# Kernel optimization log

Hardware: AMD Instinct MI355X
Metric: run time of the kernel (lower is better)

## Reference

```python
import jax, jax.numpy as jnp
import numpy as np

N_CUST = 500000
N_FUND = 50000
N_EDGE = 4000000
D_CUST = 101
D_FUND = 1
HID = 64


def setup_inputs() -> dict:
    key = jax.random.key(0)
    ks = jax.random.split(key, 16)
    s = lambda fan_in: 1.0 / np.sqrt(fan_in)
    return {
        "x_customer": jax.random.normal(ks[0], (N_CUST, D_CUST), jnp.float32),
        "x_fund": jax.random.normal(ks[1], (N_FUND, D_FUND), jnp.float32),
        "src_fund": jax.random.randint(ks[2], (N_EDGE,), 0, N_FUND, jnp.int64),
        "dst_customer": jax.random.randint(ks[3], (N_EDGE,), 0, N_CUST, jnp.int64),
        # per-node-type input projections
        "W_cust": jax.random.uniform(ks[4], (D_CUST, HID), jnp.float32, -s(D_CUST), s(D_CUST)),
        "b_cust": jax.random.uniform(ks[5], (HID,), jnp.float32, -s(D_CUST), s(D_CUST)),
        "W_fund": jax.random.uniform(ks[6], (D_FUND, HID), jnp.float32, -s(D_FUND), s(D_FUND)),
        "b_fund": jax.random.uniform(ks[7], (HID,), jnp.float32, -s(D_FUND), s(D_FUND)),
        # SAGEConv fund->customer: lin_l (neighbor aggr, bias) + lin_r (self, no bias)
        "W_l": jax.random.uniform(ks[8], (HID, HID), jnp.float32, -s(HID), s(HID)),
        "b_l": jax.random.uniform(ks[9], (HID,), jnp.float32, -s(HID), s(HID)),
        "W_r": jax.random.uniform(ks[10], (HID, HID), jnp.float32, -s(HID), s(HID)),
        # output head
        "W_out": jax.random.uniform(ks[11], (HID, 2), jnp.float32, -s(HID), s(HID)),
        "b_out": jax.random.uniform(ks[12], (2,), jnp.float32, -s(HID), s(HID)),
    }


def reference(x_customer, x_fund, src_fund, dst_customer,
              W_cust, b_cust, W_fund, b_fund, W_l, b_l, W_r, W_out, b_out):
    # per-node-type linear + relu
    h_c = jax.nn.relu(x_customer @ W_cust + b_cust)  # [N_CUST, HID]
    h_f = jax.nn.relu(x_fund @ W_fund + b_fund)      # [N_FUND, HID]

    # SAGEConv (fund -> customer): gather src fund features per edge,
    # mean-aggregate by destination customer (scatter-sum / count)
    msgs = h_f[src_fund]  # [N_EDGE, HID]
    summed = jax.ops.segment_sum(msgs, dst_customer, num_segments=N_CUST)
    cnt = jax.ops.segment_sum(jnp.ones((msgs.shape[0],), msgs.dtype),
                              dst_customer, num_segments=N_CUST)
    mean = summed / jnp.maximum(cnt, 1.0)[:, None]

    out_c = mean @ W_l + b_l + h_c @ W_r  # SAGE: lin_l(aggr) + lin_r(self)
    return out_c @ W_out + b_out          # [N_CUST, 2]
```

## Files before the change

kernel.cpp:

```cpp
#include <hip/hip_runtime.h>
#include <stdint.h>

#define N_CUST 500000
#define N_FUND 50000
#define N_EDGE 4000000
#define D_CUST 101
#define HID 64

#define NB   512
#define EPB  ((N_EDGE + NB - 1) / NB)
#define CB   1024
#define NBKT ((N_CUST + CB - 1) / CB)
#define CAP  16384
#define TILES (N_CUST / 16)

typedef float  float4u __attribute__((ext_vector_type(4), aligned(4)));
using frag_ab = __attribute__((ext_vector_type(8))) short;
using frag_cd = __attribute__((ext_vector_type(4))) float;

struct __align__(16) Accum { float g0, g1, cnt, pad; };

__device__ __forceinline__ short f2bf(float f) {
    unsigned u = __float_as_uint(f);
    u += 0x7fffu + ((u >> 16) & 1u);
    return (short)(u >> 16);
}

__global__ __launch_bounds__(256) void k_prep(
    const float* __restrict__ W_r, const float* __restrict__ W_out,
    const float* __restrict__ b_l, const float* __restrict__ b_out,
    const float* __restrict__ W_l,
    float* __restrict__ Bt, float* __restrict__ Af, float* __restrict__ c2,
    unsigned* __restrict__ gcur)
{
    int t = threadIdx.x;
    if (t < 128) {
        int h = t >> 1, j = t & 1;
        float s = 0.f, sa = 0.f;
        for (int k = 0; k < 64; ++k) {
            float wo = W_out[k * 2 + j];
            s  = fmaf(W_r[h * 64 + k], wo, s);
            sa = fmaf(W_l[h * 64 + k], wo, sa);
        }
        Bt[t] = s;
        Af[t] = sa;
    } else if (t < 130) {
        int j = t - 128;
        float s = b_out[j];
        for (int k = 0; k < 64; ++k)
            s = fmaf(b_l[k], W_out[k * 2 + j], s);
        c2[j] = s;
    }
    for (int k = t; k < NBKT; k += 256) gcur[k] = (unsigned)k * CAP;
}

__global__ __launch_bounds__(256) void k_gf(
    const float* __restrict__ x_fund,
    const float* __restrict__ W_fund,
    const float* __restrict__ b_fund,
    const float* __restrict__ Af,
    float2* __restrict__ gf)
{
    int f = blockIdx.x * 256 + threadIdx.x;
    if (f >= N_FUND) return;
    float xf = x_fund[f];
    float g0 = 0.f, g1 = 0.f;
    #pragma unroll
    for (int h = 0; h < 64; ++h) {
        float hf = fmaxf(fmaf(xf, W_fund[h], b_fund[h]), 0.f);
        g0 = fmaf(hf, Af[2 * h + 0], g0);
        g1 = fmaf(hf, Af[2 * h + 1], g1);
    }
    gf[f] = make_float2(g0, g1);
}

__global__ __launch_bounds__(256) void k_reorder(
    const int* __restrict__ src, const int* __restrict__ dst,
    unsigned* __restrict__ gcur, unsigned* __restrict__ recs)
{
    __shared__ unsigned hist[NBKT];
    __shared__ unsigned localOff[NBKT];
    __shared__ unsigned cur[NBKT];
    __shared__ unsigned baseG[NBKT];
    __shared__ unsigned ldsRec[EPB];
    __shared__ unsigned short ldsBkt[EPB];

    int t = threadIdx.x, b = blockIdx.x;
    int e0 = b * EPB, e1 = min(e0 + EPB, N_EDGE);
    int cntE = e1 - e0;

    for (int k = t; k < NBKT; k += 256) hist[k] = 0;
    __syncthreads();
    for (int e = e0 + t; e < e1; e += 256)
        atomicAdd(&hist[((unsigned)dst[e]) >> 10], 1u);
    __syncthreads();

    if (t < 64) {
        unsigned v[8], pre[8], run = 0;
        #pragma unroll
        for (int j = 0; j < 8; ++j) {
            int idx = t * 8 + j;
            v[j] = (idx < NBKT) ? hist[idx] : 0u;
            pre[j] = run; run += v[j];
        }
        unsigned sc = run;
        #pragma unroll
        for (int d = 1; d < 64; d <<= 1) {
            unsigned n = __shfl_up(sc, d, 64);
            if (t >= d) sc += n;
        }
        unsigned lane_excl = sc - run;
        #pragma unroll
        for (int j = 0; j < 8; ++j) {
            int idx = t * 8 + j;
            if (idx < NBKT) {
                localOff[idx] = lane_excl + pre[j];
                cur[idx]      = lane_excl + pre[j];
            }
        }
    }
    __syncthreads();

    for (int k = t; k < NBKT; k += 256) {
        unsigned h = hist[k];
        baseG[k] = h ? atomicAdd(&gcur[k], h) : 0u;
    }

    for (int e = e0 + t; e < e1; e += 256) {
        unsigned d = (unsigned)dst[e];
        unsigned s = (unsigned)src[e];
        unsigned k = d >> 10;
        unsigned p = atomicAdd(&cur[k], 1u);
        ldsRec[p] = s | ((d & 1023u) << 16);
        ldsBkt[p] = (unsigned short)k;
    }
    __syncthreads();

    for (int i = t; i < cntE; i += 256) {
        unsigned k = ldsBkt[i];
        unsigned g = baseG[k] + (i - localOff[k]);
        recs[g] = ldsRec[i];
    }
}

__global__ __launch_bounds__(256) void k_aggregate(
    const unsigned* __restrict__ recs, const unsigned* __restrict__ gcur,
    const float2* __restrict__ gf, float2* __restrict__ mean)
{
    __shared__ float s0[CB], s1[CB], scn[CB];
    int t = threadIdx.x, k = blockIdx.x;
    for (int c = t; c < CB; c += 256) { s0[c] = 0.f; s1[c] = 0.f; scn[c] = 0.f; }
    __syncthreads();
    unsigned r0 = (unsigned)k * CAP, r1 = gcur[k];
    for (unsigned i = r0 + t; i < r1; i += 256) {
        unsigned r = recs[i];
        float2 g = gf[r & 0xFFFFu];
        unsigned dl = r >> 16;
        atomicAdd(&s0[dl], g.x);
        atomicAdd(&s1[dl], g.y);
        atomicAdd(&scn[dl], 1.f);
    }
    __syncthreads();
    int cust0 = k * CB;
    for (int c = t; c < CB; c += 256) {
        int cu = cust0 + c;
        if (cu < N_CUST) {
            float inv = 1.0f / fmaxf(scn[c], 1.0f);
            mean[cu] = make_float2(s0[c] * inv, s1[c] * inv);
        }
    }
}

__global__ __launch_bounds__(256) void k_scatter_direct(
    const int* __restrict__ src, const int* __restrict__ dst,
    const float2* __restrict__ gf, Accum* __restrict__ A)
{
    int stride = gridDim.x * 256;
    for (int e = blockIdx.x * 256 + threadIdx.x; e < N_EDGE; e += stride) {
        int s = src[e], d = dst[e];
        float2 g = gf[s];
        unsafeAtomicAdd(&A[d].g0, g.x);
        unsafeAtomicAdd(&A[d].g1, g.y);
        unsafeAtomicAdd(&A[d].cnt, 1.0f);
    }
}

template<bool USE_MEAN>
__global__ __launch_bounds__(256) void k_cust(
    const float* __restrict__ x, const float* __restrict__ Wc,
    const float* __restrict__ bc, const float* __restrict__ Bt,
    const float* __restrict__ c2,
    const float2* __restrict__ mean, const Accum* __restrict__ A,
    float2* __restrict__ out)
{
    __shared__ float zb[4][16 * 68];
    __shared__ float sBt[128];
    int tid = threadIdx.x;
    int w = tid >> 6, lane = tid & 63;
    int c = lane & 15, q = lane >> 4;
    float* z = zb[w];

    if (tid < 128) sBt[tid] = Bt[tid];

    frag_ab bfrag[4][4];
    for (int nt = 0; nt < 4; ++nt)
        for (int kc = 0; kc < 4; ++kc) {
            frag_ab f;
            for (int j = 0; j < 8; ++j) {
                int k = kc * 32 + q * 8 + j;
                int h = nt * 16 + c;
                f[j] = (k < D_CUST) ? f2bf(Wc[k * HID + h]) : (short)0;
            }
            bfrag[nt][kc] = f;
        }
    float bcv[4];
    #pragma unroll
    for (int nt = 0; nt < 4; ++nt) bcv[nt] = bc[nt * 16 + c];
    float c20 = c2[0], c21 = c2[1];
    __syncthreads();

    int wglob = blockIdx.x * 4 + w;
    int wstride = gridDim.x * 4;
    for (int t = wglob; t < TILES; t += wstride) {
        int row = t * 16 + c;
        const float* xr = x + (size_t)row * D_CUST;
        frag_ab af[4];
        #pragma unroll
        for (int kc = 0; kc < 3; ++kc) {
            float4u lo = *(const float4u*)(xr + kc * 32 + q * 8);
            float4u hi = *(const float4u*)(xr + kc * 32 + q * 8 + 4);
            frag_ab f;
            f[0]=f2bf(lo[0]); f[1]=f2bf(lo[1]); f[2]=f2bf(lo[2]); f[3]=f2bf(lo[3]);
            f[4]=f2bf(hi[0]); f[5]=f2bf(hi[1]); f[6]=f2bf(hi[2]); f[7]=f2bf(hi[3]);
            af[kc] = f;
        }
        {
            frag_ab f = {0,0,0,0,0,0,0,0};
            if (q == 0) {
                float4u lo = *(const float4u*)(xr + 96);
                f[0]=f2bf(lo[0]); f[1]=f2bf(lo[1]); f[2]=f2bf(lo[2]); f[3]=f2bf(lo[3]);
                f[4]=f2bf(xr[100]);
            }
            af[3] = f;
        }
        frag_cd acc[4];
        #pragma unroll
        for (int nt = 0; nt < 4; ++nt)
            acc[nt] = (frag_cd){bcv[nt], bcv[nt], bcv[nt], bcv[nt]};
        #pragma unroll
        for (int kc = 0; kc < 4; ++kc)
            #pragma unroll
            for (int nt = 0; nt < 4; ++nt)
                acc[nt] = __builtin_amdgcn_mfma_f32_16x16x32_bf16(
                    af[kc], bfrag[nt][kc], acc[nt], 0, 0, 0);

        #pragma unroll
        for (int nt = 0; nt < 4; ++nt)
            #pragma unroll
            for (int i = 0; i < 4; ++i)
                z[(q * 4 + i) * 68 + nt * 16 + c] = fmaxf(acc[nt][i], 0.f);

        float p0 = 0.f, p1 = 0.f;
        #pragma unroll
        for (int j4 = 0; j4 < 4; ++j4) {
            float4u zv = *(const float4u*)(z + c * 68 + q * 16 + j4 * 4);
            float4u b0 = *(const float4u*)(sBt + q * 32 + j4 * 8);
            float4u b1 = *(const float4u*)(sBt + q * 32 + j4 * 8 + 4);
            p0 = fmaf(zv[0], b0[0], p0); p1 = fmaf(zv[0], b0[1], p1);
            p0 = fmaf(zv[1], b0[2], p0); p1 = fmaf(zv[1], b0[3], p1);
            p0 = fmaf(zv[2], b1[0], p0); p1 = fmaf(zv[2], b1[1], p1);
            p0 = fmaf(zv[3], b1[2], p0); p1 = fmaf(zv[3], b1[3], p1);
        }
        p0 += __shfl_xor(p0, 16, 64); p0 += __shfl_xor(p0, 32, 64);
        p1 += __shfl_xor(p1, 16, 64); p1 += __shfl_xor(p1, 32, 64);
        if (q == 0) {
            int orow = t * 16 + c;
            float m0, m1;
            if (USE_MEAN) {
                float2 m = mean[orow]; m0 = m.x; m1 = m.y;
            } else {
                Accum a = A[orow];
                float inv = 1.0f / fmaxf(a.cnt, 1.0f);
                m0 = a.g0 * inv; m1 = a.g1 * inv;
            }
            out[orow] = make_float2(p0 + m0 + c20, p1 + m1 + c21);
        }
    }
}

extern "C" void kernel_launch(void* const* d_in, const int* in_sizes, int n_in,
                              void* d_out, int out_size, void* d_ws, size_t ws_size,
                              hipStream_t stream) {
    const float* x_customer = (const float*)d_in[0];
    const float* x_fund     = (const float*)d_in[1];
    const int*   src_fund   = (const int*)d_in[2];
    const int*   dst_cust   = (const int*)d_in[3];
    const float* W_cust     = (const float*)d_in[4];
    const float* b_cust     = (const float*)d_in[5];
    const float* W_fund     = (const float*)d_in[6];
    const float* b_fund     = (const float*)d_in[7];
    const float* W_l        = (const float*)d_in[8];
    const float* b_l        = (const float*)d_in[9];
    const float* W_r        = (const float*)d_in[10];
    const float* W_out      = (const float*)d_in[11];
    const float* b_out      = (const float*)d_in[12];

    char* ws = (char*)d_ws;
    const size_t NEED = 4403456ull + (size_t)NBKT * CAP * 4ull + 64;

    if (ws_size >= NEED) {
        float2*   gf   = (float2*)  (ws);
        float*    Bt   = (float*)   (ws + 400000);
        float*    Af   = (float*)   (ws + 400512);
        float*    c2   = (float*)   (ws + 401024);
        unsigned* gcur = (unsigned*)(ws + 401408);
        float2*   mean = (float2*)  (ws + 403456);
        unsigned* recs = (unsigned*)(ws + 4403456);

        k_prep<<<1, 256, 0, stream>>>(W_r, W_out, b_l, b_out, W_l, Bt, Af, c2, gcur);
        k_gf<<<(N_FUND + 255) / 256, 256, 0, stream>>>(x_fund, W_fund, b_fund, Af, gf);
        k_reorder<<<NB, 256, 0, stream>>>(src_fund, dst_cust, gcur, recs);
        k_aggregate<<<NBKT, 256, 0, stream>>>(recs, gcur, gf, mean);
        k_cust<true><<<1024, 256, 0, stream>>>(
            x_customer, W_cust, b_cust, Bt, c2, mean, nullptr, (float2*)d_out);
    } else {
        Accum*    A    = (Accum*) (ws);
        float2*   gf   = (float2*)(ws + 8000000);
        float*    Bt   = (float*) (ws + 8400000);
        float*    Af   = (float*) (ws + 8400512);
        float*    c2   = (float*) (ws + 8401024);
        unsigned* gcur = (unsigned*)(ws + 8401408);

        hipMemsetAsync(A, 0, sizeof(Accum) * (size_t)N_CUST, stream);
        k_prep<<<1, 256, 0, stream>>>(W_r, W_out, b_l, b_out, W_l, Bt, Af, c2, gcur);
        k_gf<<<(N_FUND + 255) / 256, 256, 0, stream>>>(x_fund, W_fund, b_fund, Af, gf);
        k_scatter_direct<<<2048, 256, 0, stream>>>(src_fund, dst_cust, gf, A);
        k_cust<false><<<1024, 256, 0, stream>>>(
            x_customer, W_cust, b_cust, Bt, c2, nullptr, A, (float2*)d_out);
    }
}
```

Baseline: 445.3 us.

## Fuse bucket aggregation with customer MLP and fold prep into kernels

Merges the per-bucket mean aggregation into the customer projection kernel, so each block aggregates 512 customers in LDS and then computes their MFMA projection and output directly. This removes the intermediate mean buffer and its round trip through global memory. The single-block prep kernel is dropped: its weight folding is recomputed per block in k_gf and k_bucket, and the gcur initialisation becomes a memset with bucket-relative counters. Bucket size is halved to 512, which doubles the number of buckets and blocks, and each block now also reloads the W_cust fragments, adding redundant per-block setup work.

```diff
diff --git a/kernel.cpp b/kernel.cpp
--- a/kernel.cpp
+++ b/kernel.cpp
@@ -9,10 +9,10 @@
 
 #define NB   512
 #define EPB  ((N_EDGE + NB - 1) / NB)
-#define CB   1024
+#define CB   512
 #define NBKT ((N_CUST + CB - 1) / CB)
-#define CAP  16384
-#define TILES (N_CUST / 16)
+#define CAP  8192
+#define TPB  32
 
 typedef float  float4u __attribute__((ext_vector_type(4), aligned(4)));
 using frag_ab = __attribute__((ext_vector_type(8))) short;
@@ -26,50 +26,40 @@
     return (short)(u >> 16);
 }
 
-__global__ __launch_bounds__(256) void k_prep(
-    const float* __restrict__ W_r, const float* __restrict__ W_out,
-    const float* __restrict__ b_l, const float* __restrict__ b_out,
-    const float* __restrict__ W_l,
-    float* __restrict__ Bt, float* __restrict__ Af, float* __restrict__ c2,
-    unsigned* __restrict__ gcur)
-{
-    int t = threadIdx.x;
-    if (t < 128) {
-        int h = t >> 1, j = t & 1;
-        float s = 0.f, sa = 0.f;
-        for (int k = 0; k < 64; ++k) {
-            float wo = W_out[k * 2 + j];
-            s  = fmaf(W_r[h * 64 + k], wo, s);
-            sa = fmaf(W_l[h * 64 + k], wo, sa);
-        }
-        Bt[t] = s;
-        Af[t] = sa;
-    } else if (t < 130) {
-        int j = t - 128;
-        float s = b_out[j];
-        for (int k = 0; k < 64; ++k)
-            s = fmaf(b_l[k], W_out[k * 2 + j], s);
-        c2[j] = s;
-    }
-    for (int k = t; k < NBKT; k += 256) gcur[k] = (unsigned)k * CAP;
-}
-
 __global__ __launch_bounds__(256) void k_gf(
     const float* __restrict__ x_fund,
     const float* __restrict__ W_fund,
     const float* __restrict__ b_fund,
-    const float* __restrict__ Af,
+    const float* __restrict__ W_l,
+    const float* __restrict__ W_out,
     float2* __restrict__ gf)
 {
-    int f = blockIdx.x * 256 + threadIdx.x;
+    __shared__ float sAf[128];
+    __shared__ float sWf[64];
+    __shared__ float sBf[64];
+    int t = threadIdx.x;
+    if (t < 128) {
+        int h = t >> 1, j = t & 1;
+        float s = 0.f;
+        for (int k = 0; k < 64; ++k)
+            s = fmaf(W_l[h * 64 + k], W_out[k * 2 + j], s);
+        sAf[t] = s;
+    } else if (t < 192) {
+        sWf[t - 128] = W_fund[t - 128];
+    } else {
+        sBf[t - 192] = b_fund[t - 192];
+    }
+    __syncthreads();
+
+    int f = blockIdx.x * 256 + t;
     if (f >= N_FUND) return;
     float xf = x_fund[f];
     float g0 = 0.f, g1 = 0.f;
     #pragma unroll
     for (int h = 0; h < 64; ++h) {
-        float hf = fmaxf(fmaf(xf, W_fund[h], b_fund[h]), 0.f);
-        g0 = fmaf(hf, Af[2 * h + 0], g0);
-        g1 = fmaf(hf, Af[2 * h + 1], g1);
+        float hf = fmaxf(fmaf(xf, sWf[h], sBf[h]), 0.f);
+        g0 = fmaf(hf, sAf[2 * h + 0], g0);
+        g1 = fmaf(hf, sAf[2 * h + 1], g1);
     }
     gf[f] = make_float2(g0, g1);
 }
@@ -92,14 +82,14 @@
     for (int k = t; k < NBKT; k += 256) hist[k] = 0;
     __syncthreads();
     for (int e = e0 + t; e < e1; e += 256)
-        atomicAdd(&hist[((unsigned)dst[e]) >> 10], 1u);
+        atomicAdd(&hist[((unsigned)dst[e]) >> 9], 1u);
     __syncthreads();
 
     if (t < 64) {
-        unsigned v[8], pre[8], run = 0;
-        #pragma unroll
-        for (int j = 0; j < 8; ++j) {
-            int idx = t * 8 + j;
+        unsigned v[16], pre[16], run = 0;
+        #pragma unroll
+        for (int j = 0; j < 16; ++j) {
+            int idx = t * 16 + j;
             v[j] = (idx < NBKT) ? hist[idx] : 0u;
             pre[j] = run; run += v[j];
         }
@@ -111,8 +101,8 @@
         }
         unsigned lane_excl = sc - run;
         #pragma unroll
-        for (int j = 0; j < 8; ++j) {
-            int idx = t * 8 + j;
+        for (int j = 0; j < 16; ++j) {
+            int idx = t * 16 + j;
             if (idx < NBKT) {
                 localOff[idx] = lane_excl + pre[j];
                 cur[idx]      = lane_excl + pre[j];
@@ -123,15 +113,15 @@
 
     for (int k = t; k < NBKT; k += 256) {
         unsigned h = hist[k];
-        baseG[k] = h ? atomicAdd(&gcur[k], h) : 0u;
+        baseG[k] = h ? ((unsigned)k * CAP + atomicAdd(&gcur[k], h)) : 0u;
     }
 
     for (int e = e0 + t; e < e1; e += 256) {
         unsigned d = (unsigned)dst[e];
         unsigned s = (unsigned)src[e];
-        unsigned k = d >> 10;
+        unsigned k = d >> 9;
         unsigned p = atomicAdd(&cur[k], 1u);
-        ldsRec[p] = s | ((d & 1023u) << 16);
+        ldsRec[p] = s | ((d & 511u) << 16);
         ldsBkt[p] = (unsigned short)k;
     }
     __syncthreads();
@@ -143,15 +133,39 @@
     }
 }
 
-__global__ __launch_bounds__(256) void k_aggregate(
+__global__ __launch_bounds__(256) void k_bucket(
     const unsigned* __restrict__ recs, const unsigned* __restrict__ gcur,
-    const float2* __restrict__ gf, float2* __restrict__ mean)
+    const float2* __restrict__ gf,
+    const float* __restrict__ x, const float* __restrict__ Wc,
+    const float* __restrict__ bc,
+    const float* __restrict__ W_r, const float* __restrict__ W_out,
+    const float* __restrict__ b_l, const float* __restrict__ b_out,
+    float2* __restrict__ out)
 {
     __shared__ float s0[CB], s1[CB], scn[CB];
+    __shared__ float sBt[128];
+    __shared__ float sc2[2];
+    __shared__ float zb[4][16 * 68];
+
     int t = threadIdx.x, k = blockIdx.x;
+
+    if (t < 128) {
+        int h = t >> 1, j = t & 1;
+        float s = 0.f;
+        for (int kk = 0; kk < 64; ++kk)
+            s = fmaf(W_r[h * 64 + kk], W_out[kk * 2 + j], s);
+        sBt[t] = s;
+    } else if (t < 130) {
+        int j = t - 128;
+        float s = b_out[j];
+        for (int kk = 0; kk < 64; ++kk)
+            s = fmaf(b_l[kk], W_out[kk * 2 + j], s);
+        sc2[j] = s;
+    }
     for (int c = t; c < CB; c += 256) { s0[c] = 0.f; s1[c] = 0.f; scn[c] = 0.f; }
     __syncthreads();
-    unsigned r0 = (unsigned)k * CAP, r1 = gcur[k];
+
+    unsigned r0 = (unsigned)k * CAP, r1 = r0 + gcur[k];
     for (unsigned i = r0 + t; i < r1; i += 256) {
         unsigned r = recs[i];
         float2 g = gf[r & 0xFFFFu];
@@ -160,69 +174,33 @@
         atomicAdd(&s1[dl], g.y);
         atomicAdd(&scn[dl], 1.f);
     }
-    __syncthreads();
-    int cust0 = k * CB;
-    for (int c = t; c < CB; c += 256) {
-        int cu = cust0 + c;
-        if (cu < N_CUST) {
-            float inv = 1.0f / fmaxf(scn[c], 1.0f);
-            mean[cu] = make_float2(s0[c] * inv, s1[c] * inv);
-        }
-    }
-}
-
-__global__ __launch_bounds__(256) void k_scatter_direct(
-    const int* __restrict__ src, const int* __restrict__ dst,
-    const float2* __restrict__ gf, Accum* __restrict__ A)
-{
-    int stride = gridDim.x * 256;
-    for (int e = blockIdx.x * 256 + threadIdx.x; e < N_EDGE; e += stride) {
-        int s = src[e], d = dst[e];
-        float2 g = gf[s];
-        unsafeAtomicAdd(&A[d].g0, g.x);
-        unsafeAtomicAdd(&A[d].g1, g.y);
-        unsafeAtomicAdd(&A[d].cnt, 1.0f);
-    }
-}
-
-template<bool USE_MEAN>
-__global__ __launch_bounds__(256) void k_cust(
-    const float* __restrict__ x, const float* __restrict__ Wc,
-    const float* __restrict__ bc, const float* __restrict__ Bt,
-    const float* __restrict__ c2,
-    const float2* __restrict__ mean, const Accum* __restrict__ A,
-    float2* __restrict__ out)
-{
-    __shared__ float zb[4][16 * 68];
-    __shared__ float sBt[128];
-    int tid = threadIdx.x;
-    int w = tid >> 6, lane = tid & 63;
+
+    int w = t >> 6, lane = t & 63;
     int c = lane & 15, q = lane >> 4;
     float* z = zb[w];
-
-    if (tid < 128) sBt[tid] = Bt[tid];
-
     frag_ab bfrag[4][4];
     for (int nt = 0; nt < 4; ++nt)
         for (int kc = 0; kc < 4; ++kc) {
             frag_ab f;
             for (int j = 0; j < 8; ++j) {
-                int k = kc * 32 + q * 8 + j;
+                int kk = kc * 32 + q * 8 + j;
                 int h = nt * 16 + c;
-                f[j] = (k < D_CUST) ? f2bf(Wc[k * HID + h]) : (short)0;
+                f[j] = (kk < D_CUST) ? f2bf(Wc[kk * HID + h]) : (short)0;
             }
             bfrag[nt][kc] = f;
         }
     float bcv[4];
     #pragma unroll
     for (int nt = 0; nt < 4; ++nt) bcv[nt] = bc[nt * 16 + c];
-    float c20 = c2[0], c21 = c2[1];
-    __syncthreads();
-
-    int wglob = blockIdx.x * 4 + w;
-    int wstride = gridDim.x * 4;
-    for (int t = wglob; t < TILES; t += wstride) {
-        int row = t * 16 + c;
+    __syncthreads();
+
+    float c20 = sc2[0], c21 = sc2[1];
+    int cust0 = k * CB;
+    int n_tiles = min(TPB, (N_CUST - cust0) >> 4);
+
+    for (int tl = w; tl < n_tiles; tl += 4) {
+        int lrow = tl * 16 + c;
+        int row = cust0 + lrow;
         const float* xr = x + (size_t)row * D_CUST;
         frag_ab af[4];
         #pragma unroll
@@ -274,16 +252,135 @@
         p0 += __shfl_xor(p0, 16, 64); p0 += __shfl_xor(p0, 32, 64);
         p1 += __shfl_xor(p1, 16, 64); p1 += __shfl_xor(p1, 32, 64);
         if (q == 0) {
-            int orow = t * 16 + c;
-            float m0, m1;
-            if (USE_MEAN) {
-                float2 m = mean[orow]; m0 = m.x; m1 = m.y;
-            } else {
-                Accum a = A[orow];
-                float inv = 1.0f / fmaxf(a.cnt, 1.0f);
-                m0 = a.g0 * inv; m1 = a.g1 * inv;
+            float inv = 1.0f / fmaxf(scn[lrow], 1.0f);
+            out[cust0 + lrow] = make_float2(fmaf(s0[lrow], inv, p0 + c20),
+                                            fmaf(s1[lrow], inv, p1 + c21));
+        }
+    }
+}
+
+__global__ __launch_bounds__(256) void k_prep_fb(
+    const float* __restrict__ W_r, const float* __restrict__ W_out,
+    const float* __restrict__ b_l, const float* __restrict__ b_out,
+    float* __restrict__ Bt, float* __restrict__ c2)
+{
+    int t = threadIdx.x;
+    if (t < 128) {
+        int h = t >> 1, j = t & 1;
+        float s = 0.f;
+        for (int k = 0; k < 64; ++k)
+            s = fmaf(W_r[h * 64 + k], W_out[k * 2 + j], s);
+        Bt[t] = s;
+    } else if (t < 130) {
+        int j = t - 128;
+        float s = b_out[j];
+        for (int k = 0; k < 64; ++k)
+            s = fmaf(b_l[k], W_out[k * 2 + j], s);
+        c2[j] = s;
+    }
+}
+
+__global__ __launch_bounds__(256) void k_scatter_direct(
+    const int* __restrict__ src, const int* __restrict__ dst,
+    const float2* __restrict__ gf, Accum* __restrict__ A)
+{
+    int stride = gridDim.x * 256;
+    for (int e = blockIdx.x * 256 + threadIdx.x; e < N_EDGE; e += stride) {
+        int s = src[e], d = dst[e];
+        float2 g = gf[s];
+        unsafeAtomicAdd(&A[d].g0, g.x);
+        unsafeAtomicAdd(&A[d].g1, g.y);
+        unsafeAtomicAdd(&A[d].cnt, 1.0f);
+    }
+}
+
+__global__ __launch_bounds__(256) void k_cust_fb(
+    const float* __restrict__ x, const float* __restrict__ Wc,
+    const float* __restrict__ bc, const float* __restrict__ Bt,
+    const float* __restrict__ c2, const Accum* __restrict__ A,
+    float2* __restrict__ out)
+{
+    __shared__ float zb[4][16 * 68];
+    __shared__ float sBt[128];
+    int tid = threadIdx.x;
+    int w = tid >> 6, lane = tid & 63;
+    int c = lane & 15, q = lane >> 4;
+    float* z = zb[w];
+    if (tid < 128) sBt[tid] = Bt[tid];
+
+    frag_ab bfrag[4][4];
+    for (int nt = 0; nt < 4; ++nt)
+        for (int kc = 0; kc < 4; ++kc) {
+            frag_ab f;
+            for (int j = 0; j < 8; ++j) {
+                int k = kc * 32 + q * 8 + j;
+                f[j] = (k < D_CUST) ? f2bf(Wc[k * HID + nt * 16 + c]) : (short)0;
             }
-            out[orow] = make_float2(p0 + m0 + c20, p1 + m1 + c21);
+            bfrag[nt][kc] = f;
+        }
+    float bcv[4];
+    #pragma unroll
+    for (int nt = 0; nt < 4; ++nt) bcv[nt] = bc[nt * 16 + c];
+    float c20 = c2[0], c21 = c2[1];
+    __syncthreads();
+
+    int wglob = blockIdx.x * 4 + w;
+    int wstride = gridDim.x * 4;
+    for (int t = wglob; t < N_CUST / 16; t += wstride) {
+        int row = t * 16 + c;
+        const float* xr = x + (size_t)row * D_CUST;
+        frag_ab af[4];
+        #pragma unroll
+        for (int kc = 0; kc < 3; ++kc) {
+            float4u lo = *(const float4u*)(xr + kc * 32 + q * 8);
+            float4u hi = *(const float4u*)(xr + kc * 32 + q * 8 + 4);
+            frag_ab f;
+            f[0]=f2bf(lo[0]); f[1]=f2bf(lo[1]); f[2]=f2bf(lo[2]); f[3]=f2bf(lo[3]);
+            f[4]=f2bf(hi[0]); f[5]=f2bf(hi[1]); f[6]=f2bf(hi[2]); f[7]=f2bf(hi[3]);
+            af[kc] = f;
+        }
+        {
+            frag_ab f = {0,0,0,0,0,0,0,0};
+            if (q == 0) {
+                float4u lo = *(const float4u*)(xr + 96);
+                f[0]=f2bf(lo[0]); f[1]=f2bf(lo[1]); f[2]=f2bf(lo[2]); f[3]=f2bf(lo[3]);
+                f[4]=f2bf(xr[100]);
+            }
+            af[3] = f;
+        }
+        frag_cd acc[4];
+        #pragma unroll
+        for (int nt = 0; nt < 4; ++nt)
+            acc[nt] = (frag_cd){bcv[nt], bcv[nt], bcv[nt], bcv[nt]};
+        #pragma unroll
+        for (int kc = 0; kc < 4; ++kc)
+            #pragma unroll
+            for (int nt = 0; nt < 4; ++nt)
+                acc[nt] = __builtin_amdgcn_mfma_f32_16x16x32_bf16(
+                    af[kc], bfrag[nt][kc], acc[nt], 0, 0, 0);
+        #pragma unroll
+        for (int nt = 0; nt < 4; ++nt)
+            #pragma unroll
+            for (int i = 0; i < 4; ++i)
+                z[(q * 4 + i) * 68 + nt * 16 + c] = fmaxf(acc[nt][i], 0.f);
+        float p0 = 0.f, p1 = 0.f;
+        #pragma unroll
+        for (int j4 = 0; j4 < 4; ++j4) {
+            float4u zv = *(const float4u*)(z + c * 68 + q * 16 + j4 * 4);
+            float4u b0 = *(const float4u*)(sBt + q * 32 + j4 * 8);
+            float4u b1 = *(const float4u*)(sBt + q * 32 + j4 * 8 + 4);
+            p0 = fmaf(zv[0], b0[0], p0); p1 = fmaf(zv[0], b0[1], p1);
+            p0 = fmaf(zv[1], b0[2], p0); p1 = fmaf(zv[1], b0[3], p1);
+            p0 = fmaf(zv[2], b1[0], p0); p1 = fmaf(zv[2], b1[1], p1);
+            p0 = fmaf(zv[3], b1[2], p0); p1 = fmaf(zv[3], b1[3], p1);
+        }
+        p0 += __shfl_xor(p0, 16, 64); p0 += __shfl_xor(p0, 32, 64);
+        p1 += __shfl_xor(p1, 16, 64); p1 += __shfl_xor(p1, 32, 64);
+        if (q == 0) {
+            Accum a = A[t * 16 + c];
+            float inv = 1.0f / fmaxf(a.cnt, 1.0f);
+            out[t * 16 + c] = make_float2(fmaf(a.g0, inv, p0 + c20),
+                                          fmaf(a.g1, inv, p1 + c21));
         }
     }
 }
@@ -306,36 +403,32 @@
     const float* b_out      = (const float*)d_in[12];
 
     char* ws = (char*)d_ws;
-    const size_t NEED = 4403456ull + (size_t)NBKT * CAP * 4ull + 64;
+    const size_t NEED = 404096ull + (size_t)NBKT * CAP * 4ull;
 
     if (ws_size >= NEED) {
         float2*   gf   = (float2*)  (ws);
-        float*    Bt   = (float*)   (ws + 400000);
-        float*    Af   = (float*)   (ws + 400512);
-        float*    c2   = (float*)   (ws + 401024);
-        unsigned* gcur = (unsigned*)(ws + 401408);
-        float2*   mean = (float2*)  (ws + 403456);
-        unsigned* recs = (unsigned*)(ws + 4403456);
-
-        k_prep<<<1, 256, 0, stream>>>(W_r, W_out, b_l, b_out, W_l, Bt, Af, c2, gcur);
-        k_gf<<<(N_FUND + 255) / 256, 256, 0, stream>>>(x_fund, W_fund, b_fund, Af, gf);
+        unsigned* gcur = (unsigned*)(ws + 400000);
+        unsigned* recs = (unsigned*)(ws + 404096);
+
+        hipMemsetAsync(gcur, 0, NBKT * sizeof(unsigned), stream);
+        k_gf<<<(N_FUND + 255) / 256, 256, 0, stream>>>(
+            x_fund, W_fund, b_fund, W_l, W_out, gf);
         k_reorder<<<NB, 256, 0, stream>>>(src_fund, dst_cust, gcur, recs);
-        k_aggregate<<<NBKT, 256, 0, stream>>>(recs, gcur, gf, mean);
-        k_cust<true><<<1024, 256, 0, stream>>>(
-            x_customer, W_cust, b_cust, Bt, c2, mean, nullptr, (float2*)d_out);
+        k_bucket<<<NBKT, 256, 0, stream>>>(
+            recs, gcur, gf, x_customer, W_cust, b_cust,
+            W_r, W_out, b_l, b_out, (float2*)d_out);
     } else {
-        Accum*    A    = (Accum*) (ws);
-        float2*   gf   = (float2*)(ws + 8000000);
-        float*    Bt   = (float*) (ws + 8400000);
-        float*    Af   = (float*) (ws + 8400512);
-        float*    c2   = (float*) (ws + 8401024);
-        unsigned* gcur = (unsigned*)(ws + 8401408);
+        Accum*  A  = (Accum*) (ws);
+        float2* gf = (float2*)(ws + 8000000);
+        float*  Bt = (float*) (ws + 8400000);
+        float*  c2 = (float*) (ws + 8400512);
 
         hipMemsetAsync(A, 0, sizeof(Accum) * (size_t)N_CUST, stream);
-        k_prep<<<1, 256, 0, stream>>>(W_r, W_out, b_l, b_out, W_l, Bt, Af, c2, gcur);
-        k_gf<<<(N_FUND + 255) / 256, 256, 0, stream>>>(x_fund, W_fund, b_fund, Af, gf);
+        k_prep_fb<<<1, 256, 0, stream>>>(W_r, W_out, b_l, b_out, Bt, c2);
+        k_gf<<<(N_FUND + 255) / 256, 256, 0, stream>>>(
+            x_fund, W_fund, b_fund, W_l, W_out, gf);
         k_scatter_direct<<<2048, 256, 0, stream>>>(src_fund, dst_cust, gf, A);
-        k_cust<false><<<1024, 256, 0, stream>>>(
-            x_customer, W_cust, b_cust, Bt, c2, nullptr, A, (float2*)d_out);
-    }
-}
+        k_cust_fb<<<1024, 256, 0, stream>>>(
+            x_customer, W_cust, b_cust, Bt, c2, A, (float2*)d_out);
+    }
+}
```

After: 425.5 us. 1.05x faster.
